# Kernel optimization log

Measured on AMD Instinct MI355X. Metric: run time of the kernel, lower is better.

The kernel has to match this reference:

```python
import jax, jax.numpy as jnp
import numpy as np


def _safe_norm(x, eps=1e-8):
    return jnp.sqrt(jnp.clip(jnp.sum(x * x, axis=-1, keepdims=True), eps))


def _normalize(x, eps=1e-8):
    return x / _safe_norm(x, eps)


def _safe_direction(primary, fallback, eps=1e-6):
    bad = _safe_norm(primary, eps) < eps  # [N,1] bool
    out = jnp.where(bad, fallback, primary)
    return _normalize(out, eps)


def _build_frames(x):
    # x: [N,3] (N >= 2). Returns per-node rotation frames [N,3,3] (columns = axes).
    d = x[1:] - x[:-1]
    prev = jnp.concatenate([d[:1], d], axis=0)
    nxt = jnp.concatenate([d, d[-1:]], axis=0)
    tangent = _safe_direction(prev + nxt, nxt)
    curvature = _safe_direction(nxt - prev, prev)
    ay_raw = curvature - tangent * jnp.sum(curvature * tangent, axis=-1, keepdims=True)
    ay = _safe_direction(ay_raw, jnp.cross(tangent, prev))
    az = _safe_direction(jnp.cross(tangent, ay), jnp.cross(tangent, curvature))
    ay = _safe_direction(jnp.cross(az, tangent), ay)
    return jnp.stack([tangent, ay, az], axis=-1)


def setup_inputs() -> dict:
    key = jax.random.key(0)
    N, H, EH = 1024, 256, 128  # EH = max(16, H//2)
    ks = jax.random.split(key, 16)

    def lin(k, fi, fo):
        k1, k2 = jax.random.split(k)
        lim = 1.0 / np.sqrt(fi)
        W = jax.random.uniform(k1, (fi, fo), minval=-lim, maxval=lim, dtype=jnp.float32)
        b = jax.random.uniform(k2, (fo,), minval=-lim, maxval=lim, dtype=jnp.float32)
        return W, b

    h = jax.random.normal(ks[0], (N, H), dtype=jnp.float32)
    x_cond = jnp.cumsum(jax.random.normal(ks[1], (N, 3), dtype=jnp.float32) * 1.5, axis=0)
    x_t = x_cond + 0.05 * jax.random.normal(ks[2], (N, 3), dtype=jnp.float32)
    tau = jax.random.uniform(ks[3], (1,), dtype=jnp.float32)
    W_np1, b_np1 = lin(ks[4], H + 6, H)
    W_np2, b_np2 = lin(ks[5], H, H)
    w_src, b_src = lin(ks[6], H, 1)
    w_dst, b_dst = lin(ks[7], H, 1)
    w_ns, b_ns = lin(ks[8], H, 1)
    W_eg1, b_eg1 = lin(ks[9], 4, EH)
    w_eg2, b_eg2 = lin(ks[10], EH, 1)
    W_out1, b_out1 = lin(ks[11], H + 6, H)
    W_out2, b_out2 = lin(ks[12], H, 3)
    return dict(h=h, x_t=x_t, x_cond=x_cond, tau=tau,
                W_np1=W_np1, b_np1=b_np1, W_np2=W_np2, b_np2=b_np2,
                w_src=w_src, b_src=b_src, w_dst=w_dst, b_dst=b_dst,
                w_ns=w_ns, b_ns=b_ns, W_eg1=W_eg1, b_eg1=b_eg1,
                w_eg2=w_eg2, b_eg2=b_eg2, W_out1=W_out1, b_out1=b_out1,
                W_out2=W_out2, b_out2=b_out2)


def reference(h, x_t, x_cond, tau,
              W_np1, b_np1, W_np2, b_np2,
              w_src, b_src, w_dst, b_dst,
              w_ns, b_ns, W_eg1, b_eg1, w_eg2, b_eg2,
              W_out1, b_out1, W_out2, b_out2):
    silu = jax.nn.silu
    n = x_t.shape[0]
    frames = _build_frames(x_cond)                       # [N,3,3]
    delta = x_t - x_cond
    delta_local = jnp.einsum('nji,nj->ni', frames, delta)  # frames^T @ delta
    t = tau.reshape(())
    t_emb = jnp.broadcast_to(jnp.stack([t, jnp.sin(t), jnp.cos(t)]), (n, 3))
    node_feat = jnp.concatenate([h, delta_local, t_emb], axis=-1)
    nh = silu(node_feat @ W_np1 + b_np1)
    nh = silu(nh @ W_np2 + b_np2)                        # [N,H]
    # pairwise local geometry: rel[n,m] = x[m] - x[n], rotated into node n's frame
    rel = x_t[None, :, :] - x_t[:, None, :]              # [N,N,3]
    rel_local = jnp.einsum('nji,nmj->nmi', frames, rel)  # [N,N,3]
    dist = jnp.linalg.norm(rel_local, axis=-1, keepdims=True)
    edge_feat = jnp.concatenate([rel_local, dist], axis=-1)  # [N,N,4]
    eh = silu(edge_feat @ W_eg1 + b_eg1)                 # [N,N,EH]
    edge_logit = (eh @ w_eg2 + b_eg2)[..., 0]            # [N,N]
    src = nh @ w_src + b_src                             # [N,1] -> broadcast over m
    dst = (nh @ w_dst + b_dst)[:, 0]                     # [N]
    logits = src + dst[None, :] + edge_logit             # [N,N]
    diag = jnp.eye(n, dtype=bool)
    logits = jnp.where(diag, -10000.0, logits)
    attn = jax.nn.softmax(logits, axis=1)
    attn = jnp.where(diag, 0.0, attn)
    attn = attn / jnp.clip(jnp.sum(attn, axis=1, keepdims=True), 1e-6)
    ns = jax.nn.sigmoid(nh @ w_ns + b_ns)[:, 0]          # [N]
    msgs = jnp.einsum('nm,m,nmi->ni', attn, ns, rel_local)  # [N,3]
    uf = jnp.concatenate([nh, delta_local, msgs], axis=-1)
    local_update = silu(uf @ W_out1 + b_out1) @ W_out2 + b_out2
    vel_local = local_update + 0.25 * msgs
    return jnp.einsum('nij,nj->ni', frames, vel_local)
```

## Files before the change

### kernel.cpp

```cpp
#include <hip/hip_runtime.h>
#include <math.h>

#define DEV __device__ __forceinline__

struct F3 { float x, y, z; };

DEV F3 mkf3(float x, float y, float z){ F3 r; r.x=x; r.y=y; r.z=z; return r; }
DEV F3 f3add(F3 a, F3 b){ return mkf3(a.x+b.x, a.y+b.y, a.z+b.z); }
DEV F3 f3sub(F3 a, F3 b){ return mkf3(a.x-b.x, a.y-b.y, a.z-b.z); }
DEV F3 f3scale(F3 a, float s){ return mkf3(a.x*s, a.y*s, a.z*s); }
DEV float f3dot(F3 a, F3 b){ return a.x*b.x + a.y*b.y + a.z*b.z; }
DEV F3 f3cross(F3 a, F3 b){
  return mkf3(a.y*b.z - a.z*b.y, a.z*b.x - a.x*b.z, a.x*b.y - a.y*b.x);
}
DEV F3 f3dir(F3 v){
  float ss = f3dot(v, v);
  float inv = 1.0f / sqrtf(fmaxf(ss, 1e-6f));
  return f3scale(v, inv);
}
DEV float fast_silu(float x){
  return x * __builtin_amdgcn_rcpf(1.0f + __expf(-x));
}
DEV float fast_sigmoid(float x){
  return __builtin_amdgcn_rcpf(1.0f + __expf(-x));
}

__global__ void frames_kernel(const float* __restrict__ xc,
                              const float* __restrict__ xt,
                              float* __restrict__ frames,
                              float* __restrict__ dl, int N)
{
  int n = blockIdx.x * blockDim.x + threadIdx.x;
  if (n >= N) return;
  int pn = (n > 0) ? n - 1 : 0;
  int qn = (n < N - 1) ? n : N - 2;
  F3 prev = mkf3(xc[(pn+1)*3+0]-xc[pn*3+0], xc[(pn+1)*3+1]-xc[pn*3+1], xc[(pn+1)*3+2]-xc[pn*3+2]);
  F3 nxt  = mkf3(xc[(qn+1)*3+0]-xc[qn*3+0], xc[(qn+1)*3+1]-xc[qn*3+1], xc[(qn+1)*3+2]-xc[qn*3+2]);

  F3 tangent = f3dir(f3add(prev, nxt));
  F3 curv    = f3dir(f3sub(nxt, prev));
  float ct   = f3dot(curv, tangent);
  F3 ay      = f3dir(f3sub(curv, f3scale(tangent, ct)));
  F3 az      = f3dir(f3cross(tangent, ay));
  ay         = f3dir(f3cross(az, tangent));

  float* fr = frames + n * 9;
  fr[0] = tangent.x; fr[1] = ay.x; fr[2] = az.x;
  fr[3] = tangent.y; fr[4] = ay.y; fr[5] = az.y;
  fr[6] = tangent.z; fr[7] = ay.z; fr[8] = az.z;

  F3 delta = mkf3(xt[n*3+0]-xc[n*3+0], xt[n*3+1]-xc[n*3+1], xt[n*3+2]-xc[n*3+2]);
  dl[n*3+0] = f3dot(tangent, delta);
  dl[n*3+1] = f3dot(ay, delta);
  dl[n*3+2] = f3dot(az, delta);
}

__global__ __launch_bounds__(256) void node_mlp(
    const float* __restrict__ h, const float* __restrict__ dl,
    const float* __restrict__ tau,
    const float* __restrict__ W1, const float* __restrict__ b1,
    const float* __restrict__ W2, const float* __restrict__ b2,
    const float* __restrict__ w_src, const float* __restrict__ b_src,
    const float* __restrict__ w_dst, const float* __restrict__ b_dst,
    const float* __restrict__ w_ns, const float* __restrict__ b_ns,
    float* __restrict__ nh, float* __restrict__ srcv,
    float* __restrict__ dstv, float* __restrict__ nsv, int N)
{
  const int n0 = blockIdx.x * 4, tid = threadIdx.x;
  __shared__ float4 fA[262];
  __shared__ float4 fB[256];
  __shared__ float red[4][4][3];

  {
    const float* hp = h + n0 * 256 + tid;
    fA[tid] = make_float4(hp[0], hp[256], hp[512], hp[768]);
  }
  if (tid < 6) {
    int k = 256 + tid;
    float4 v;
    if (tid < 3) {
      v = make_float4(dl[(n0+0)*3+tid], dl[(n0+1)*3+tid],
                      dl[(n0+2)*3+tid], dl[(n0+3)*3+tid]);
    } else {
      float t = tau[0];
      float s = (tid == 3) ? t : ((tid == 4) ? sinf(t) : cosf(t));
      v = make_float4(s, s, s, s);
    }
    fA[k] = v;
  }
  __syncthreads();

  {
    float bb = b1[tid];
    float a0 = bb, a1 = bb, a2 = bb, a3 = bb;
    const float* Wp = W1 + tid;
    for (int kb = 0; kb < 256; kb += 64) {
      float w[64];
      #pragma unroll
      for (int u = 0; u < 64; ++u) w[u] = Wp[(kb + u) * 256];
      #pragma unroll
      for (int u = 0; u < 64; ++u) {
        float4 f = fA[kb + u];
        a0 = fmaf(f.x, w[u], a0); a1 = fmaf(f.y, w[u], a1);
        a2 = fmaf(f.z, w[u], a2); a3 = fmaf(f.w, w[u], a3);
      }
    }
    #pragma unroll
    for (int k = 256; k < 262; ++k) {
      float w = Wp[k * 256];
      float4 f = fA[k];
      a0 = fmaf(f.x, w, a0); a1 = fmaf(f.y, w, a1);
      a2 = fmaf(f.z, w, a2); a3 = fmaf(f.w, w, a3);
    }
    fB[tid] = make_float4(fast_silu(a0), fast_silu(a1), fast_silu(a2), fast_silu(a3));
  }
  __syncthreads();

  float bb = b2[tid];
  float a0 = bb, a1 = bb, a2 = bb, a3 = bb;
  const float* Wp = W2 + tid;
  for (int kb = 0; kb < 256; kb += 64) {
    float w[64];
    #pragma unroll
    for (int u = 0; u < 64; ++u) w[u] = Wp[(kb + u) * 256];
    #pragma unroll
    for (int u = 0; u < 64; ++u) {
      float4 f = fB[kb + u];
      a0 = fmaf(f.x, w[u], a0); a1 = fmaf(f.y, w[u], a1);
      a2 = fmaf(f.z, w[u], a2); a3 = fmaf(f.w, w[u], a3);
    }
  }

  const float wsv = w_src[tid], wdv = w_dst[tid], wnv = w_ns[tid];
  const int wave = tid >> 6, lane = tid & 63;
  float va[4] = {fast_silu(a0), fast_silu(a1), fast_silu(a2), fast_silu(a3)};
  #pragma unroll
  for (int r = 0; r < 4; ++r) {
    nh[(n0 + r) * 256 + tid] = va[r];
    float ps = va[r] * wsv, pd = va[r] * wdv, pn = va[r] * wnv;
    for (int off = 32; off; off >>= 1) {
      ps += __shfl_down(ps, off);
      pd += __shfl_down(pd, off);
      pn += __shfl_down(pn, off);
    }
    if (lane == 0) { red[wave][r][0] = ps; red[wave][r][1] = pd; red[wave][r][2] = pn; }
  }
  __syncthreads();
  if (tid < 4) {
    int r = tid;
    float s0 = 0.f, s1 = 0.f, s2 = 0.f;
    #pragma unroll
    for (int w = 0; w < 4; ++w) { s0 += red[w][r][0]; s1 += red[w][r][1]; s2 += red[w][r][2]; }
    srcv[n0 + r] = s0 + b_src[0];
    dstv[n0 + r] = s1 + b_dst[0];
    nsv[n0 + r]  = fast_sigmoid(s2 + b_ns[0]);
  }
}

__global__ __launch_bounds__(256, 8) void edge_softmax(
    const float* __restrict__ x_t, const float* __restrict__ frames,
    const float* __restrict__ srcv, const float* __restrict__ dstv,
    const float* __restrict__ nsv,
    const float* __restrict__ W_eg1, const float* __restrict__ b_eg1,
    const float* __restrict__ w_eg2, const float* __restrict__ b_eg2,
    float* __restrict__ msgs, int N)
{
  const int n = blockIdx.x, tid = threadIdx.x;
  __shared__ float redmax[4];
  __shared__ float red[4][4];

  const float f0 = frames[n*9+0], f1 = frames[n*9+1], f2 = frames[n*9+2],
              f3_ = frames[n*9+3], f4 = frames[n*9+4], f5 = frames[n*9+5],
              f6 = frames[n*9+6], f7 = frames[n*9+7], f8 = frames[n*9+8];
  const float x0 = x_t[n*3+0], x1 = x_t[n*3+1], x2 = x_t[n*3+2];
  const float sn = srcv[n];
  const float b2v = b_eg2[0];

  const float nl2e = -1.44269504088896340736f;
  const float nln2 = -0.69314718055994530942f;

  float ds0[4], ds1[4], ds2[4], ds3[4];
  #pragma unroll
  for (int e = 0; e < 4; ++e) {
    const int m = e * 256 + tid;
    float rx = x_t[m * 3 + 0] - x0;
    float ry = x_t[m * 3 + 1] - x1;
    float rz = x_t[m * 3 + 2] - x2;
    float rl0 = f0 * rx + f3_ * ry + f6 * rz;
    float rl1 = f1 * rx + f4 * ry + f7 * rz;
    float rl2 = f2 * rx + f5 * ry + f8 * rz;
    float dist = sqrtf(rl0 * rl0 + rl1 * rl1 + rl2 * rl2);
    ds0[e] = nl2e * rl0; ds1[e] = nl2e * rl1;
    ds2[e] = nl2e * rl2; ds3[e] = nl2e * dist;
  }

  float acc[4] = {0.f, 0.f, 0.f, 0.f};
  #pragma unroll 8
  for (int j = 0; j < 128; ++j) {
    const float wx = W_eg1[j];
    const float wy = W_eg1[128 + j];
    const float wz = W_eg1[256 + j];
    const float wd = W_eg1[384 + j];
    const float bj = b_eg1[j];
    const float w2 = w_eg2[j];
    const float bs = bj * nl2e;
    #pragma unroll
    for (int e = 0; e < 4; ++e) {
      float tp = fmaf(wd, ds3[e], bs);
      tp = fmaf(wz, ds2[e], tp);
      tp = fmaf(wy, ds1[e], tp);
      tp = fmaf(wx, ds0[e], tp);
      float ex = __builtin_amdgcn_exp2f(tp);
      float sg = __builtin_amdgcn_rcpf(1.0f + ex);
      acc[e] = fmaf(w2, tp * sg, acc[e]);
    }
  }

  float l[4];
  float lmax = -3.4e38f;
  #pragma unroll
  for (int e = 0; e < 4; ++e) {
    const int m = e * 256 + tid;
    float lg = sn + dstv[m] + b2v + nln2 * acc[e];
    if (m == n) lg = -10000.0f;
    l[e] = lg;
    lmax = fmaxf(lmax, lg);
  }

  for (int off = 32; off; off >>= 1) lmax = fmaxf(lmax, __shfl_down(lmax, off));
  const int wave = tid >> 6, lane = tid & 63;
  if (lane == 0) redmax[wave] = lmax;
  __syncthreads();
  const float mx = fmaxf(fmaxf(redmax[0], redmax[1]), fmaxf(redmax[2], redmax[3]));

  float sum = 0.f, a0 = 0.f, a1 = 0.f, a2 = 0.f;
  #pragma unroll
  for (int e = 0; e < 4; ++e) {
    const int m = e * 256 + tid;
    float ee = __expf(l[e] - mx);
    sum += ee;
    float w = ee * nsv[m];
    a0 = fmaf(w, ds0[e] * nln2, a0);
    a1 = fmaf(w, ds1[e] * nln2, a1);
    a2 = fmaf(w, ds2[e] * nln2, a2);
  }
  for (int off = 32; off; off >>= 1) {
    sum += __shfl_down(sum, off);
    a0 += __shfl_down(a0, off);
    a1 += __shfl_down(a1, off);
    a2 += __shfl_down(a2, off);
  }
  if (lane == 0) { red[wave][0] = sum; red[wave][1] = a0; red[wave][2] = a1; red[wave][3] = a2; }
  __syncthreads();
  if (tid == 0) {
    float Z = red[0][0] + red[1][0] + red[2][0] + red[3][0];
    float m0 = red[0][1] + red[1][1] + red[2][1] + red[3][1];
    float m1 = red[0][2] + red[1][2] + red[2][2] + red[3][2];
    float m2 = red[0][3] + red[1][3] + red[2][3] + red[3][3];
    float invZ = 1.0f / Z;
    msgs[n * 3 + 0] = m0 * invZ;
    msgs[n * 3 + 1] = m1 * invZ;
    msgs[n * 3 + 2] = m2 * invZ;
  }
}

__global__ __launch_bounds__(256) void out_mlp(
    const float* __restrict__ nh, const float* __restrict__ dl,
    const float* __restrict__ msgs, const float* __restrict__ frames,
    const float* __restrict__ W1, const float* __restrict__ b1,
    const float* __restrict__ W2, const float* __restrict__ b2,
    float* __restrict__ out, int N)
{
  const int n0 = blockIdx.x * 4, tid = threadIdx.x;
  __shared__ float4 feat4[262];
  __shared__ float red[4][4][3];
  {
    const float* hp = nh + n0 * 256 + tid;
    feat4[tid] = make_float4(hp[0], hp[256], hp[512], hp[768]);
  }
  if (tid < 6) {
    int k = 256 + tid;
    float4 v;
    if (tid < 3) {
      v = make_float4(dl[(n0+0)*3+tid], dl[(n0+1)*3+tid],
                      dl[(n0+2)*3+tid], dl[(n0+3)*3+tid]);
    } else {
      int c = tid - 3;
      v = make_float4(msgs[(n0+0)*3+c], msgs[(n0+1)*3+c],
                      msgs[(n0+2)*3+c], msgs[(n0+3)*3+c]);
    }
    feat4[k] = v;
  }
  __syncthreads();

  float bb = b1[tid];
  float a0 = bb, a1 = bb, a2 = bb, a3 = bb;
  const float* Wp = W1 + tid;
  for (int kb = 0; kb < 256; kb += 64) {
    float w[64];
    #pragma unroll
    for (int u = 0; u < 64; ++u) w[u] = Wp[(kb + u) * 256];
    #pragma unroll
    for (int u = 0; u < 64; ++u) {
      float4 f = feat4[kb + u];
      a0 = fmaf(f.x, w[u], a0); a1 = fmaf(f.y, w[u], a1);
      a2 = fmaf(f.z, w[u], a2); a3 = fmaf(f.w, w[u], a3);
    }
  }
  #pragma unroll
  for (int k = 256; k < 262; ++k) {
    float w = Wp[k * 256];
    float4 f = feat4[k];
    a0 = fmaf(f.x, w, a0); a1 = fmaf(f.y, w, a1);
    a2 = fmaf(f.z, w, a2); a3 = fmaf(f.w, w, a3);
  }

  const float w0 = W2[tid * 3 + 0], w1 = W2[tid * 3 + 1], w2 = W2[tid * 3 + 2];
  const int wave = tid >> 6, lane = tid & 63;
  float va[4] = {fast_silu(a0), fast_silu(a1), fast_silu(a2), fast_silu(a3)};
  #pragma unroll
  for (int r = 0; r < 4; ++r) {
    float p0 = va[r] * w0, p1 = va[r] * w1, p2 = va[r] * w2;
    for (int off = 32; off; off >>= 1) {
      p0 += __shfl_down(p0, off);
      p1 += __shfl_down(p1, off);
      p2 += __shfl_down(p2, off);
    }
    if (lane == 0) { red[wave][r][0] = p0; red[wave][r][1] = p1; red[wave][r][2] = p2; }
  }
  __syncthreads();
  if (tid < 4) {
    int r = tid, n = n0 + r;
    float s0 = 0.f, s1 = 0.f, s2 = 0.f;
    #pragma unroll
    for (int w = 0; w < 4; ++w) { s0 += red[w][r][0]; s1 += red[w][r][1]; s2 += red[w][r][2]; }
    float m0 = msgs[n * 3 + 0], m1 = msgs[n * 3 + 1], m2 = msgs[n * 3 + 2];
    float v0 = s0 + b2[0] + 0.25f * m0;
    float v1 = s1 + b2[1] + 0.25f * m1;
    float v2 = s2 + b2[2] + 0.25f * m2;
    const float* fr = frames + n * 9;
    out[n * 3 + 0] = fr[0] * v0 + fr[1] * v1 + fr[2] * v2;
    out[n * 3 + 1] = fr[3] * v0 + fr[4] * v1 + fr[5] * v2;
    out[n * 3 + 2] = fr[6] * v0 + fr[7] * v1 + fr[8] * v2;
  }
}

extern "C" void kernel_launch(void* const* d_in, const int* in_sizes, int n_in,
                              void* d_out, int out_size, void* d_ws, size_t ws_size,
                              hipStream_t stream) {
  const float* h      = (const float*)d_in[0];
  const float* x_t    = (const float*)d_in[1];
  const float* x_cond = (const float*)d_in[2];
  const float* tau    = (const float*)d_in[3];
  const float* W_np1  = (const float*)d_in[4];
  const float* b_np1  = (const float*)d_in[5];
  const float* W_np2  = (const float*)d_in[6];
  const float* b_np2  = (const float*)d_in[7];
  const float* w_src  = (const float*)d_in[8];
  const float* b_src  = (const float*)d_in[9];
  const float* w_dst  = (const float*)d_in[10];
  const float* b_dst  = (const float*)d_in[11];
  const float* w_ns   = (const float*)d_in[12];
  const float* b_ns   = (const float*)d_in[13];
  const float* W_eg1  = (const float*)d_in[14];
  const float* b_eg1  = (const float*)d_in[15];
  const float* w_eg2  = (const float*)d_in[16];
  const float* b_eg2  = (const float*)d_in[17];
  const float* W_out1 = (const float*)d_in[18];
  const float* b_out1 = (const float*)d_in[19];
  const float* W_out2 = (const float*)d_in[20];
  const float* b_out2 = (const float*)d_in[21];
  float* out = (float*)d_out;

  const int N = in_sizes[1] / 3;

  float* ws     = (float*)d_ws;
  float* frames = ws;
  float* dl     = frames + N * 9;
  float* nh     = dl + N * 3;
  float* srcv   = nh + N * 256;
  float* dstv   = srcv + N;
  float* nsv    = dstv + N;
  float* msgs   = nsv + N;

  frames_kernel<<<(N + 255) / 256, 256, 0, stream>>>(x_cond, x_t, frames, dl, N);
  node_mlp<<<N / 4, 256, 0, stream>>>(h, dl, tau, W_np1, b_np1, W_np2, b_np2,
                                      w_src, b_src, w_dst, b_dst, w_ns, b_ns,
                                      nh, srcv, dstv, nsv, N);
  edge_softmax<<<N, 256, 0, stream>>>(x_t, frames, srcv, dstv, nsv,
                                      W_eg1, b_eg1, w_eg2, b_eg2, msgs, N);
  out_mlp<<<N / 4, 256, 0, stream>>>(nh, dl, msgs, frames,
                                     W_out1, b_out1, W_out2, b_out2, out, N);
}
```

Baseline: 66.29 us.

## Split edge softmax across two blocks per node and prepack edge weights

The edge softmax kernel now runs two blocks per node, each covering half of the neighbours. Each block writes a partial max, partial sum and partial messages, and out_mlp merges the two halves with a log-sum-exp style combine. The edge MLP weights are prescaled by the exp2/ln2 constants and packed into float4 pairs in an extra frames_kernel block, which cuts per-iteration loads and multiplies. This doubles the grid for better occupancy and latency hiding, at the cost of extra partial-result traffic and a merge step.

After: 67.18 us. Within noise of the previous version (+1.3%).

```diff
diff --git a/kernel.cpp b/kernel.cpp
--- a/kernel.cpp
+++ b/kernel.cpp
@@ -28,8 +28,27 @@
 __global__ void frames_kernel(const float* __restrict__ xc,
                               const float* __restrict__ xt,
                               float* __restrict__ frames,
-                              float* __restrict__ dl, int N)
+                              float* __restrict__ dl,
+                              const float* __restrict__ W_eg1,
+                              const float* __restrict__ b_eg1,
+                              const float* __restrict__ w_eg2,
+                              float* __restrict__ wpk, int N)
 {
+  if (blockIdx.x == (unsigned)(N / 256)) {
+    int j = threadIdx.x;
+    if (j < 128) {
+      const float nl2e = -1.44269504088896340736f;
+      const float nln2 = -0.69314718055994530942f;
+      wpk[j*8+0] = nl2e * W_eg1[j];
+      wpk[j*8+1] = nl2e * W_eg1[128 + j];
+      wpk[j*8+2] = nl2e * W_eg1[256 + j];
+      wpk[j*8+3] = nl2e * W_eg1[384 + j];
+      wpk[j*8+4] = nl2e * b_eg1[j];
+      wpk[j*8+5] = nln2 * w_eg2[j];
+      wpk[j*8+6] = 0.f; wpk[j*8+7] = 0.f;
+    }
+    return;
+  }
   int n = blockIdx.x * blockDim.x + threadIdx.x;
   if (n >= N) return;
   int pn = (n > 0) ? n - 1 : 0;
@@ -161,11 +180,12 @@
     const float* __restrict__ x_t, const float* __restrict__ frames,
     const float* __restrict__ srcv, const float* __restrict__ dstv,
     const float* __restrict__ nsv,
-    const float* __restrict__ W_eg1, const float* __restrict__ b_eg1,
-    const float* __restrict__ w_eg2, const float* __restrict__ b_eg2,
-    float* __restrict__ msgs, int N)
+    const float* __restrict__ wpk, const float* __restrict__ b_eg2,
+    float* __restrict__ part, int N)
 {
-  const int n = blockIdx.x, tid = threadIdx.x;
+  const int bid = blockIdx.x;
+  const int n = bid >> 1, half = bid & 1;
+  const int tid = threadIdx.x;
   __shared__ float redmax[4];
   __shared__ float red[4][4];
 
@@ -175,53 +195,46 @@
   const float x0 = x_t[n*3+0], x1 = x_t[n*3+1], x2 = x_t[n*3+2];
   const float sn = srcv[n];
   const float b2v = b_eg2[0];
-
-  const float nl2e = -1.44269504088896340736f;
-  const float nln2 = -0.69314718055994530942f;
-
-  float ds0[4], ds1[4], ds2[4], ds3[4];
-  #pragma unroll
-  for (int e = 0; e < 4; ++e) {
-    const int m = e * 256 + tid;
+  const int m0i = half * 512 + tid;
+
+  float r0[2], r1[2], r2[2], dd[2];
+  #pragma unroll
+  for (int e = 0; e < 2; ++e) {
+    const int m = m0i + e * 256;
     float rx = x_t[m * 3 + 0] - x0;
     float ry = x_t[m * 3 + 1] - x1;
     float rz = x_t[m * 3 + 2] - x2;
-    float rl0 = f0 * rx + f3_ * ry + f6 * rz;
-    float rl1 = f1 * rx + f4 * ry + f7 * rz;
-    float rl2 = f2 * rx + f5 * ry + f8 * rz;
-    float dist = sqrtf(rl0 * rl0 + rl1 * rl1 + rl2 * rl2);
-    ds0[e] = nl2e * rl0; ds1[e] = nl2e * rl1;
-    ds2[e] = nl2e * rl2; ds3[e] = nl2e * dist;
-  }
-
-  float acc[4] = {0.f, 0.f, 0.f, 0.f};
+    r0[e] = f0 * rx + f3_ * ry + f6 * rz;
+    r1[e] = f1 * rx + f4 * ry + f7 * rz;
+    r2[e] = f2 * rx + f5 * ry + f8 * rz;
+    dd[e] = sqrtf(r0[e]*r0[e] + r1[e]*r1[e] + r2[e]*r2[e]);
+  }
+
+  const float4* wp4 = (const float4*)wpk;
+  float acc[2] = {0.f, 0.f};
   #pragma unroll 8
   for (int j = 0; j < 128; ++j) {
-    const float wx = W_eg1[j];
-    const float wy = W_eg1[128 + j];
-    const float wz = W_eg1[256 + j];
-    const float wd = W_eg1[384 + j];
-    const float bj = b_eg1[j];
-    const float w2 = w_eg2[j];
-    const float bs = bj * nl2e;
-    #pragma unroll
-    for (int e = 0; e < 4; ++e) {
-      float tp = fmaf(wd, ds3[e], bs);
-      tp = fmaf(wz, ds2[e], tp);
-      tp = fmaf(wy, ds1[e], tp);
-      tp = fmaf(wx, ds0[e], tp);
+    const float4 wa = wp4[2*j];
+    const float4 wb = wp4[2*j+1];
+    #pragma unroll
+    for (int e = 0; e < 2; ++e) {
+      float tp = fmaf(wa.w, dd[e], wb.x);
+      tp = fmaf(wa.z, r2[e], tp);
+      tp = fmaf(wa.y, r1[e], tp);
+      tp = fmaf(wa.x, r0[e], tp);
+      float q  = tp * wb.y;
       float ex = __builtin_amdgcn_exp2f(tp);
       float sg = __builtin_amdgcn_rcpf(1.0f + ex);
-      acc[e] = fmaf(w2, tp * sg, acc[e]);
-    }
-  }
-
-  float l[4];
+      acc[e] = fmaf(q, sg, acc[e]);
+    }
+  }
+
+  float l[2];
   float lmax = -3.4e38f;
   #pragma unroll
-  for (int e = 0; e < 4; ++e) {
-    const int m = e * 256 + tid;
-    float lg = sn + dstv[m] + b2v + nln2 * acc[e];
+  for (int e = 0; e < 2; ++e) {
+    const int m = m0i + e * 256;
+    float lg = sn + dstv[m] + b2v + acc[e];
     if (m == n) lg = -10000.0f;
     l[e] = lg;
     lmax = fmaxf(lmax, lg);
@@ -235,14 +248,14 @@
 
   float sum = 0.f, a0 = 0.f, a1 = 0.f, a2 = 0.f;
   #pragma unroll
-  for (int e = 0; e < 4; ++e) {
-    const int m = e * 256 + tid;
+  for (int e = 0; e < 2; ++e) {
+    const int m = m0i + e * 256;
     float ee = __expf(l[e] - mx);
     sum += ee;
     float w = ee * nsv[m];
-    a0 = fmaf(w, ds0[e] * nln2, a0);
-    a1 = fmaf(w, ds1[e] * nln2, a1);
-    a2 = fmaf(w, ds2[e] * nln2, a2);
+    a0 = fmaf(w, r0[e], a0);
+    a1 = fmaf(w, r1[e], a1);
+    a2 = fmaf(w, r2[e], a2);
   }
   for (int off = 32; off; off >>= 1) {
     sum += __shfl_down(sum, off);
@@ -257,16 +270,14 @@
     float m0 = red[0][1] + red[1][1] + red[2][1] + red[3][1];
     float m1 = red[0][2] + red[1][2] + red[2][2] + red[3][2];
     float m2 = red[0][3] + red[1][3] + red[2][3] + red[3][3];
-    float invZ = 1.0f / Z;
-    msgs[n * 3 + 0] = m0 * invZ;
-    msgs[n * 3 + 1] = m1 * invZ;
-    msgs[n * 3 + 2] = m2 * invZ;
+    float* p = part + bid * 8;
+    p[0] = mx; p[1] = Z; p[2] = m0; p[3] = m1; p[4] = m2;
   }
 }
 
 __global__ __launch_bounds__(256) void out_mlp(
     const float* __restrict__ nh, const float* __restrict__ dl,
-    const float* __restrict__ msgs, const float* __restrict__ frames,
+    const float* __restrict__ part, const float* __restrict__ frames,
     const float* __restrict__ W1, const float* __restrict__ b1,
     const float* __restrict__ W2, const float* __restrict__ b2,
     float* __restrict__ out, int N)
@@ -274,10 +285,23 @@
   const int n0 = blockIdx.x * 4, tid = threadIdx.x;
   __shared__ float4 feat4[262];
   __shared__ float red[4][4][3];
+  __shared__ float smsg[4][3];
   {
     const float* hp = nh + n0 * 256 + tid;
     feat4[tid] = make_float4(hp[0], hp[256], hp[512], hp[768]);
   }
+  if (tid < 4) {
+    int n = n0 + tid;
+    const float* p0 = part + (2*n) * 8;
+    const float* p1 = part + (2*n+1) * 8;
+    float mx = fmaxf(p0[0], p1[0]);
+    float s0 = __expf(p0[0] - mx), s1 = __expf(p1[0] - mx);
+    float invZ = 1.0f / (p0[1]*s0 + p1[1]*s1);
+    smsg[tid][0] = (p0[2]*s0 + p1[2]*s1) * invZ;
+    smsg[tid][1] = (p0[3]*s0 + p1[3]*s1) * invZ;
+    smsg[tid][2] = (p0[4]*s0 + p1[4]*s1) * invZ;
+  }
+  __syncthreads();
   if (tid < 6) {
     int k = 256 + tid;
     float4 v;
@@ -286,8 +310,7 @@
                       dl[(n0+2)*3+tid], dl[(n0+3)*3+tid]);
     } else {
       int c = tid - 3;
-      v = make_float4(msgs[(n0+0)*3+c], msgs[(n0+1)*3+c],
-                      msgs[(n0+2)*3+c], msgs[(n0+3)*3+c]);
+      v = make_float4(smsg[0][c], smsg[1][c], smsg[2][c], smsg[3][c]);
     }
     feat4[k] = v;
   }
@@ -334,7 +357,7 @@
     float s0 = 0.f, s1 = 0.f, s2 = 0.f;
     #pragma unroll
     for (int w = 0; w < 4; ++w) { s0 += red[w][r][0]; s1 += red[w][r][1]; s2 += red[w][r][2]; }
-    float m0 = msgs[n * 3 + 0], m1 = msgs[n * 3 + 1], m2 = msgs[n * 3 + 2];
+    float m0 = smsg[r][0], m1 = smsg[r][1], m2 = smsg[r][2];
     float v0 = s0 + b2[0] + 0.25f * m0;
     float v1 = s1 + b2[1] + 0.25f * m1;
     float v2 = s2 + b2[2] + 0.25f * m2;
@@ -381,14 +404,16 @@
   float* srcv   = nh + N * 256;
   float* dstv   = srcv + N;
   float* nsv    = dstv + N;
-  float* msgs   = nsv + N;
-
-  frames_kernel<<<(N + 255) / 256, 256, 0, stream>>>(x_cond, x_t, frames, dl, N);
+  float* part   = nsv + N;
+  float* wpk    = part + 2 * N * 8;
+
+  frames_kernel<<<N / 256 + 1, 256, 0, stream>>>(x_cond, x_t, frames, dl,
+                                                 W_eg1, b_eg1, w_eg2, wpk, N);
   node_mlp<<<N / 4, 256, 0, stream>>>(h, dl, tau, W_np1, b_np1, W_np2, b_np2,
                                       w_src, b_src, w_dst, b_dst, w_ns, b_ns,
                                       nh, srcv, dstv, nsv, N);
-  edge_softmax<<<N, 256, 0, stream>>>(x_t, frames, srcv, dstv, nsv,
-                                      W_eg1, b_eg1, w_eg2, b_eg2, msgs, N);
-  out_mlp<<<N / 4, 256, 0, stream>>>(nh, dl, msgs, frames,
+  edge_softmax<<<2 * N, 256, 0, stream>>>(x_t, frames, srcv, dstv, nsv,
+                                          wpk, b_eg2, part, N);
+  out_mlp<<<N / 4, 256, 0, stream>>>(nh, dl, part, frames,
                                      W_out1, b_out1, W_out2, b_out2, out, N);
 }
```

## Prepack scaled edge-MLP weights and use packed float2 math in edge softmax

Applied to the files above, without the earlier changes.

An extra block in the frames kernel prescales the edge-gate weights by -log2(e) and -ln(2) and interleaves them into 8-float records, so edge_softmax reads them as float4 with explicit prefetch of the next chunk. The inner loop works on two-wide vector types to encourage packed FMA instructions, and the per-edge prescaling multiplies are removed. The launch-bounds occupancy hint is dropped. In exchange it adds workspace, a dependency on N being divisible by 256 for the packing block, and a prefetch that reads past the 128 records into a zero-padded tail.

Result: no change. 65.07 us (-1.8%).

```diff
diff --git a/kernel.cpp b/kernel.cpp
--- a/kernel.cpp
+++ b/kernel.cpp
@@ -2,6 +2,9 @@
 #include <math.h>
 
 #define DEV __device__ __forceinline__
+
+typedef float v2f __attribute__((ext_vector_type(2)));
+DEV v2f splat2(float s){ return (v2f){s, s}; }
 
 struct F3 { float x, y, z; };
 
@@ -28,8 +31,29 @@
 __global__ void frames_kernel(const float* __restrict__ xc,
                               const float* __restrict__ xt,
                               float* __restrict__ frames,
-                              float* __restrict__ dl, int N)
+                              float* __restrict__ dl,
+                              const float* __restrict__ W_eg1,
+                              const float* __restrict__ b_eg1,
+                              const float* __restrict__ w_eg2,
+                              float* __restrict__ wpk, int N)
 {
+  if (blockIdx.x == (unsigned)(N / 256)) {
+    int j = threadIdx.x;
+    if (j < 128) {
+      const float nl2e = -1.44269504088896340736f;
+      const float nln2 = -0.69314718055994530942f;
+      wpk[j*8+0] = nl2e * W_eg1[j];
+      wpk[j*8+1] = nl2e * W_eg1[128 + j];
+      wpk[j*8+2] = nl2e * W_eg1[256 + j];
+      wpk[j*8+3] = nl2e * W_eg1[384 + j];
+      wpk[j*8+4] = nl2e * b_eg1[j];
+      wpk[j*8+5] = nln2 * w_eg2[j];
+      wpk[j*8+6] = 0.f; wpk[j*8+7] = 0.f;
+    } else if (j < 144) {
+      wpk[1024 + (j - 128)] = 0.f;
+    }
+    return;
+  }
   int n = blockIdx.x * blockDim.x + threadIdx.x;
   if (n >= N) return;
   int pn = (n > 0) ? n - 1 : 0;
@@ -157,12 +181,11 @@
   }
 }
 
-__global__ __launch_bounds__(256, 8) void edge_softmax(
+__global__ __launch_bounds__(256) void edge_softmax(
     const float* __restrict__ x_t, const float* __restrict__ frames,
     const float* __restrict__ srcv, const float* __restrict__ dstv,
     const float* __restrict__ nsv,
-    const float* __restrict__ W_eg1, const float* __restrict__ b_eg1,
-    const float* __restrict__ w_eg2, const float* __restrict__ b_eg2,
+    const float* __restrict__ wpk, const float* __restrict__ b_eg2,
     float* __restrict__ msgs, int N)
 {
   const int n = blockIdx.x, tid = threadIdx.x;
@@ -176,52 +199,68 @@
   const float sn = srcv[n];
   const float b2v = b_eg2[0];
 
-  const float nl2e = -1.44269504088896340736f;
-  const float nln2 = -0.69314718055994530942f;
-
-  float ds0[4], ds1[4], ds2[4], ds3[4];
+  float r0s[4], r1s[4], r2s[4], dds[4];
   #pragma unroll
   for (int e = 0; e < 4; ++e) {
     const int m = e * 256 + tid;
     float rx = x_t[m * 3 + 0] - x0;
     float ry = x_t[m * 3 + 1] - x1;
     float rz = x_t[m * 3 + 2] - x2;
-    float rl0 = f0 * rx + f3_ * ry + f6 * rz;
-    float rl1 = f1 * rx + f4 * ry + f7 * rz;
-    float rl2 = f2 * rx + f5 * ry + f8 * rz;
-    float dist = sqrtf(rl0 * rl0 + rl1 * rl1 + rl2 * rl2);
-    ds0[e] = nl2e * rl0; ds1[e] = nl2e * rl1;
-    ds2[e] = nl2e * rl2; ds3[e] = nl2e * dist;
-  }
-
-  float acc[4] = {0.f, 0.f, 0.f, 0.f};
-  #pragma unroll 8
-  for (int j = 0; j < 128; ++j) {
-    const float wx = W_eg1[j];
-    const float wy = W_eg1[128 + j];
-    const float wz = W_eg1[256 + j];
-    const float wd = W_eg1[384 + j];
-    const float bj = b_eg1[j];
-    const float w2 = w_eg2[j];
-    const float bs = bj * nl2e;
-    #pragma unroll
-    for (int e = 0; e < 4; ++e) {
-      float tp = fmaf(wd, ds3[e], bs);
-      tp = fmaf(wz, ds2[e], tp);
-      tp = fmaf(wy, ds1[e], tp);
-      tp = fmaf(wx, ds0[e], tp);
-      float ex = __builtin_amdgcn_exp2f(tp);
-      float sg = __builtin_amdgcn_rcpf(1.0f + ex);
-      acc[e] = fmaf(w2, tp * sg, acc[e]);
-    }
-  }
+    r0s[e] = f0 * rx + f3_ * ry + f6 * rz;
+    r1s[e] = f1 * rx + f4 * ry + f7 * rz;
+    r2s[e] = f2 * rx + f5 * ry + f8 * rz;
+    dds[e] = sqrtf(r0s[e]*r0s[e] + r1s[e]*r1s[e] + r2s[e]*r2s[e]);
+  }
+  const v2f r0A = {r0s[0], r0s[1]}, r0B = {r0s[2], r0s[3]};
+  const v2f r1A = {r1s[0], r1s[1]}, r1B = {r1s[2], r1s[3]};
+  const v2f r2A = {r2s[0], r2s[1]}, r2B = {r2s[2], r2s[3]};
+  const v2f ddA = {dds[0], dds[1]}, ddB = {dds[2], dds[3]};
+
+  v2f accA = {0.f, 0.f}, accB = {0.f, 0.f};
+
+  const float4* __restrict__ wp4 = (const float4*)wpk;
+
+#define J_STEP(WA, WB)                                                    \
+  {                                                                       \
+    v2f tpA = splat2(WB.x) + splat2(WA.w) * ddA;                          \
+    tpA += splat2(WA.z) * r2A;                                            \
+    tpA += splat2(WA.y) * r1A;                                            \
+    tpA += splat2(WA.x) * r0A;                                            \
+    v2f tpB = splat2(WB.x) + splat2(WA.w) * ddB;                          \
+    tpB += splat2(WA.z) * r2B;                                            \
+    tpB += splat2(WA.y) * r1B;                                            \
+    tpB += splat2(WA.x) * r0B;                                            \
+    v2f eA, eB;                                                           \
+    eA.x = __builtin_amdgcn_exp2f(tpA.x); eA.y = __builtin_amdgcn_exp2f(tpA.y); \
+    eB.x = __builtin_amdgcn_exp2f(tpB.x); eB.y = __builtin_amdgcn_exp2f(tpB.y); \
+    v2f opA = eA + splat2(1.0f);                                          \
+    v2f opB = eB + splat2(1.0f);                                          \
+    v2f sgA, sgB;                                                         \
+    sgA.x = __builtin_amdgcn_rcpf(opA.x); sgA.y = __builtin_amdgcn_rcpf(opA.y); \
+    sgB.x = __builtin_amdgcn_rcpf(opB.x); sgB.y = __builtin_amdgcn_rcpf(opB.y); \
+    accA += (splat2(WB.y) * tpA) * sgA;                                   \
+    accB += (splat2(WB.y) * tpB) * sgB;                                   \
+  }
+
+  float4 ca0 = wp4[0], cb0 = wp4[1], ca1 = wp4[2], cb1 = wp4[3];
+  for (int c = 0; c < 64; ++c) {
+    float4 na0 = wp4[(c + 1) * 4 + 0];
+    float4 nb0 = wp4[(c + 1) * 4 + 1];
+    float4 na1 = wp4[(c + 1) * 4 + 2];
+    float4 nb1 = wp4[(c + 1) * 4 + 3];
+    J_STEP(ca0, cb0)
+    J_STEP(ca1, cb1)
+    ca0 = na0; cb0 = nb0; ca1 = na1; cb1 = nb1;
+  }
+#undef J_STEP
 
   float l[4];
   float lmax = -3.4e38f;
+  float accs[4] = {accA.x, accA.y, accB.x, accB.y};
   #pragma unroll
   for (int e = 0; e < 4; ++e) {
     const int m = e * 256 + tid;
-    float lg = sn + dstv[m] + b2v + nln2 * acc[e];
+    float lg = sn + dstv[m] + b2v + accs[e];
     if (m == n) lg = -10000.0f;
     l[e] = lg;
     lmax = fmaxf(lmax, lg);
@@ -233,6 +272,9 @@
   __syncthreads();
   const float mx = fmaxf(fmaxf(redmax[0], redmax[1]), fmaxf(redmax[2], redmax[3]));
 
+  float r0all[4] = {r0A.x, r0A.y, r0B.x, r0B.y};
+  float r1all[4] = {r1A.x, r1A.y, r1B.x, r1B.y};
+  float r2all[4] = {r2A.x, r2A.y, r2B.x, r2B.y};
   float sum = 0.f, a0 = 0.f, a1 = 0.f, a2 = 0.f;
   #pragma unroll
   for (int e = 0; e < 4; ++e) {
@@ -240,9 +282,9 @@
     float ee = __expf(l[e] - mx);
     sum += ee;
     float w = ee * nsv[m];
-    a0 = fmaf(w, ds0[e] * nln2, a0);
-    a1 = fmaf(w, ds1[e] * nln2, a1);
-    a2 = fmaf(w, ds2[e] * nln2, a2);
+    a0 = fmaf(w, r0all[e], a0);
+    a1 = fmaf(w, r1all[e], a1);
+    a2 = fmaf(w, r2all[e], a2);
   }
   for (int off = 32; off; off >>= 1) {
     sum += __shfl_down(sum, off);
@@ -253,7 +295,7 @@
   if (lane == 0) { red[wave][0] = sum; red[wave][1] = a0; red[wave][2] = a1; red[wave][3] = a2; }
   __syncthreads();
   if (tid == 0) {
-    float Z = red[0][0] + red[1][0] + red[2][0] + red[3][0];
+    float Z  = red[0][0] + red[1][0] + red[2][0] + red[3][0];
     float m0 = red[0][1] + red[1][1] + red[2][1] + red[3][1];
     float m1 = red[0][2] + red[1][2] + red[2][2] + red[3][2];
     float m2 = red[0][3] + red[1][3] + red[2][3] + red[3][3];
@@ -382,13 +424,15 @@
   float* dstv   = srcv + N;
   float* nsv    = dstv + N;
   float* msgs   = nsv + N;
-
-  frames_kernel<<<(N + 255) / 256, 256, 0, stream>>>(x_cond, x_t, frames, dl, N);
+  float* wpk    = msgs + N * 3;
+
+  frames_kernel<<<N / 256 + 1, 256, 0, stream>>>(x_cond, x_t, frames, dl,
+                                                 W_eg1, b_eg1, w_eg2, wpk, N);
   node_mlp<<<N / 4, 256, 0, stream>>>(h, dl, tau, W_np1, b_np1, W_np2, b_np2,
                                       w_src, b_src, w_dst, b_dst, w_ns, b_ns,
                                       nh, srcv, dstv, nsv, N);
   edge_softmax<<<N, 256, 0, stream>>>(x_t, frames, srcv, dstv, nsv,
-                                      W_eg1, b_eg1, w_eg2, b_eg2, msgs, N);
+                                      wpk, b_eg2, msgs, N);
   out_mlp<<<N / 4, 256, 0, stream>>>(nh, dl, msgs, frames,
                                      W_out1, b_out1, W_out2, b_out2, out, N);
 }
```
